# Optimization experiments

Hardware: AMD Instinct MI355X
Metric: run time of the kernel (lower is better)

The kernel has to match this reference:

```python
import jax, jax.numpy as jnp
import numpy as np
from jax import lax

N, D, H, E = 8192, 1024, 4096, 8


def setup_inputs() -> dict:
    key = jax.random.key(0)
    ks = jax.random.split(key, 4)
    return {
        "x": jax.random.normal(ks[0], (N, D), dtype=jnp.float32),
        "wg": jax.random.normal(ks[1], (D, E), dtype=jnp.float32) * 0.001,
        "fc1_w": jax.random.normal(ks[2], (E, D, H), dtype=jnp.float32) * 0.001,
        "fc1_b": jnp.zeros((E, 1, H), dtype=jnp.float32),
        "fc2_w": jax.random.normal(ks[3], (E, H, D), dtype=jnp.float32) * 0.001,
        "fc2_b": jnp.zeros((E, 1, D), dtype=jnp.float32),
        "k": 2,
    }


def reference(x, wg, fc1_w, fc1_b, fc2_w, fc2_b, k):
    n, d = x.shape
    e = wg.shape[1]
    cap = (k * n) // e  # expert capacity (capacity factor 1.0)

    # --- gate ---
    scores = jax.nn.softmax(x @ wg, axis=-1)          # [N,E]
    topv, topi = lax.top_k(scores, k)                 # [N,k]

    # --- top-k routing: position of each (token, slot) within its expert buffer ---
    masks = jax.nn.one_hot(topi, e, dtype=jnp.int32)  # [N,k,E]
    # slot-major priority: all slot-0 assignments before slot-1
    m = jnp.transpose(masks, (1, 0, 2)).reshape(k * n, e)
    pos_flat = jnp.cumsum(m, axis=0) - m              # position before own assignment
    pos = jnp.sum(pos_flat * m, axis=1).reshape(k, n).T   # [N,k]
    valid = pos < cap                                  # capacity overflow -> dropped

    # --- load-balance aux loss (top-1 fraction * mean gate prob) ---
    me = scores.mean(axis=0)                           # [E]
    ce = masks[:, 0, :].astype(scores.dtype).mean(axis=0)
    l_aux = e * jnp.sum(me * ce)

    # --- encode (dispatch): scatter tokens into [E, C, D] buffers ---
    w = valid.astype(x.dtype)                          # [N,k]
    flat_idx = topi * cap + jnp.where(valid, pos, 0)   # [N,k]
    contrib = (x[:, None, :] * w[:, :, None]).reshape(-1, d)
    dispatched = jnp.zeros((e * cap, d), x.dtype).at[flat_idx.reshape(-1)].add(contrib)
    dispatched = dispatched.reshape(e, cap, d)

    # --- batched expert FFN (all-to-all is identity on one device) ---
    h = jax.nn.relu(jnp.einsum('ecd,edh->ech', dispatched, fc1_w) + fc1_b)
    y = jnp.einsum('ech,ehd->ecd', h, fc2_w) + fc2_b   # [E,C,D]

    # --- decode (combine): gather back and weight by gate scores ---
    gathered = y.reshape(e * cap, d)[flat_idx]         # [N,k,D]
    output = jnp.einsum('nk,nkd->nd', topv * w, gathered)
    return output, l_aux
```

## Files before the change

kernel.cpp:

```cpp
#include <hip/hip_runtime.h>
#include <hip/hip_bf16.h>
#include <stdint.h>

#define N_TOK 8192
#define DMODEL 1024
#define HDIM 4096
#define NEXP 8
#define CAP 2048
#define GATE_BLOCKS (N_TOK / 4)

typedef float floatx4 __attribute__((ext_vector_type(4)));
typedef int int32x4_t __attribute__((ext_vector_type(4)));
typedef int int32x8_t __attribute__((ext_vector_type(8)));

static __device__ __forceinline__ void async_copy16(const void* g, void* l) {
  __builtin_amdgcn_global_load_lds(
      (const __attribute__((address_space(1))) void*)g,
      (__attribute__((address_space(3))) void*)l, 16, 0, 0);
}

static __device__ __forceinline__ unsigned int pk4_fp8(float a, float b, float c, float d) {
  int r = __builtin_amdgcn_cvt_pk_fp8_f32(a, b, 0, 0);
  r = __builtin_amdgcn_cvt_pk_fp8_f32(c, d, r, 1);
  return (unsigned int)r;
}

__global__ __launch_bounds__(256) void gate_kernel(
    const float* __restrict__ x, const float* __restrict__ wg,
    float* __restrict__ topv, int* __restrict__ topi,
    float* __restrict__ me_part, int* __restrict__ ce_part) {
  __shared__ float sm_p[4][NEXP];
  __shared__ int sm_i0[4];
  int wave = threadIdx.x >> 6;
  int lane = threadIdx.x & 63;
  int n = blockIdx.x * 4 + wave;
  float acc[NEXP];
#pragma unroll
  for (int e = 0; e < NEXP; e++) acc[e] = 0.f;
  const float* xr = x + (size_t)n * DMODEL;
#pragma unroll 4
  for (int i = 0; i < DMODEL / 64; i++) {
    int idx = lane + 64 * i;
    float xv = xr[idx];
    const float4* wr = (const float4*)(wg + (size_t)idx * NEXP);
    float4 w0 = wr[0], w1 = wr[1];
    acc[0] += xv * w0.x; acc[1] += xv * w0.y;
    acc[2] += xv * w0.z; acc[3] += xv * w0.w;
    acc[4] += xv * w1.x; acc[5] += xv * w1.y;
    acc[6] += xv * w1.z; acc[7] += xv * w1.w;
  }
#pragma unroll
  for (int e = 0; e < NEXP; e++) {
    float v = acc[e];
#pragma unroll
    for (int off = 32; off > 0; off >>= 1) v += __shfl_down(v, off, 64);
    acc[e] = v;
  }
  if (lane == 0) {
    float mx = acc[0];
#pragma unroll
    for (int e = 1; e < NEXP; e++) mx = fmaxf(mx, acc[e]);
    float p[NEXP]; float s = 0.f;
#pragma unroll
    for (int e = 0; e < NEXP; e++) { p[e] = expf(acc[e] - mx); s += p[e]; }
    float inv = 1.f / s;
#pragma unroll
    for (int e = 0; e < NEXP; e++) p[e] *= inv;
    int i0 = 0; float v0 = p[0];
#pragma unroll
    for (int e = 1; e < NEXP; e++) if (p[e] > v0) { v0 = p[e]; i0 = e; }
    int i1 = -1; float v1 = -1.f;
#pragma unroll
    for (int e = 0; e < NEXP; e++) {
      if (e == i0) continue;
      if (p[e] > v1) { v1 = p[e]; i1 = e; }
    }
    topv[n * 2] = v0; topv[n * 2 + 1] = v1;
    topi[n * 2] = i0; topi[n * 2 + 1] = i1;
#pragma unroll
    for (int e = 0; e < NEXP; e++) sm_p[wave][e] = p[e];
    sm_i0[wave] = i0;
  }
  __syncthreads();
  if (threadIdx.x < NEXP) {
    int e = threadIdx.x;
    float pm = 0.f; int cc = 0;
#pragma unroll
    for (int w = 0; w < 4; w++) {
      pm += sm_p[w][e];
      cc += (sm_i0[w] == e) ? 1 : 0;
    }
    me_part[blockIdx.x * NEXP + e] = pm;
    ce_part[blockIdx.x * NEXP + e] = cc;
  }
}

__global__ __launch_bounds__(1024) void scan_kernel(
    const int* __restrict__ topi, const float* __restrict__ topv,
    int* __restrict__ flat_idx, float* __restrict__ cw) {
  __shared__ int hist[16][NEXP];
  __shared__ int base[NEXP];
  int tid = threadIdx.x;
  int w = tid >> 6, lane = tid & 63;
  if (tid < NEXP) base[tid] = 0;
  int vals[16];
#pragma unroll
  for (int c = 0; c < 16; c++) {
    int j = c * 1024 + tid;
    vals[c] = topi[(size_t)(j & 8191) * 2 + (j >> 13)];
  }
  __syncthreads();
  for (int c = 0; c < 16; c++) {
    int j = c * 1024 + tid;
    int slot = j >> 13;
    int n = j & 8191;
    int e = vals[c];
    int rank = 0;
#pragma unroll
    for (int ee = 0; ee < NEXP; ee++) {
      unsigned long long m = __ballot(e == ee);
      if (e == ee) rank = __popcll(m & ((1ull << lane) - 1ull));
      if (lane == ee) hist[w][ee] = __popcll(m);
    }
    __syncthreads();
    if (tid < NEXP) {
      int run = base[tid];
#pragma unroll
      for (int ww = 0; ww < 16; ww++) {
        int t = hist[ww][tid];
        hist[ww][tid] = run;
        run += t;
      }
      base[tid] = run;
    }
    __syncthreads();
    int pos = hist[w][e] + rank;
    bool valid = pos < CAP;
    flat_idx[n * 2 + slot] = e * CAP + (valid ? pos : 0);
    cw[n * 2 + slot] = valid ? topv[n * 2 + slot] : 0.f;
    __syncthreads();
  }
}

__global__ __launch_bounds__(256) void transpose_cvt_fp8(
    const float* __restrict__ in, unsigned char* __restrict__ out,
    int R, int C) {
  __shared__ float tile[32][129];
  const float* inp = in + (size_t)blockIdx.z * R * C;
  unsigned char* outp = out + (size_t)blockIdx.z * R * C;
  int c0 = blockIdx.x * 32, r0 = blockIdx.y * 128;
  int t = threadIdx.x;
#pragma unroll
  for (int p = 0; p < 4; p++) {
    int r = p * 32 + (t >> 3);
    int c4 = (t & 7) * 4;
    float4 v = *(const float4*)(inp + (size_t)(r0 + r) * C + c0 + c4);
    tile[c4 + 0][r] = v.x; tile[c4 + 1][r] = v.y;
    tile[c4 + 2][r] = v.z; tile[c4 + 3][r] = v.w;
  }
  __syncthreads();
  int c = t >> 3, r16 = (t & 7) * 16;
  unsigned int w[4];
#pragma unroll
  for (int j = 0; j < 4; j++) {
    float a = tile[c][r16 + j * 4 + 0] * 512.f;
    float b = tile[c][r16 + j * 4 + 1] * 512.f;
    float cc2 = tile[c][r16 + j * 4 + 2] * 512.f;
    float d = tile[c][r16 + j * 4 + 3] * 512.f;
    w[j] = pk4_fp8(a, b, cc2, d);
  }
  uint4 o; o.x = w[0]; o.y = w[1]; o.z = w[2]; o.w = w[3];
  *(uint4*)(outp + (size_t)(c0 + c) * R + r0 + r16) = o;
}

__global__ __launch_bounds__(64) void dispatch_kernel(
    const float* __restrict__ x, const int* __restrict__ flat_idx,
    const float* __restrict__ cw, unsigned char* __restrict__ disp) {
  int a = blockIdx.x;
  if (cw[a] == 0.f) return;
  int n = a >> 1;
  int f = flat_idx[a];
  int lane = threadIdx.x;
  const float4* xr = (const float4*)(x + (size_t)n * DMODEL);
  unsigned int* dr = (unsigned int*)(disp + (size_t)f * DMODEL);
#pragma unroll
  for (int i = 0; i < 4; i++) {
    float4 v = xr[lane + 64 * i];
    dr[lane + 64 * i] = pk4_fp8(v.x, v.y, v.z, v.w);
  }
}

template <int K_DIM, bool RELU, bool OUT_FP8>
__global__ __launch_bounds__(256) void gemm_fp8_kernel(
    const unsigned char* __restrict__ A, const unsigned char* __restrict__ BT,
    const float* __restrict__ bias, void* __restrict__ Cout, int M, int Ncols,
    float inv_scale, float out_mult) {
  constexpr int BK = 128;
  __shared__ unsigned char As[128 * BK];
  __shared__ unsigned char Bs[128 * BK];
  int e = blockIdx.z;
  int tn = blockIdx.x, tm = blockIdx.y;
  const unsigned char* Ae = A + (size_t)e * M * K_DIM + (size_t)tm * 128 * K_DIM;
  const unsigned char* Be = BT + (size_t)e * Ncols * K_DIM + (size_t)tn * 128 * K_DIM;
  int wv = threadIdx.x >> 6, l = threadIdx.x & 63;
  int wm = wv >> 1, wn = wv & 1;
  int l15 = l & 15, quad = l >> 4;
  int rbase = wv * 8 + (l >> 3);
  int cg = (l & 7) ^ ((l >> 3) & 7);
  floatx4 acc[4][4] = {};
  for (int k0 = 0; k0 < K_DIM; k0 += BK) {
#pragma unroll
    for (int i = 0; i < 4; i++) {
      int r = rbase + i * 32;
      async_copy16(Ae + (size_t)r * K_DIM + k0 + cg * 16, As + i * 4096 + wv * 1024);
      async_copy16(Be + (size_t)r * K_DIM + k0 + cg * 16, Bs + i * 4096 + wv * 1024);
    }
    __syncthreads();
    int32x8_t af[4], bf[4];
#pragma unroll
    for (int mi = 0; mi < 4; mi++) {
      int m = wm * 64 + mi * 16 + l15;
      int x0 = (quad * 2) ^ (m & 7), x1 = (quad * 2 + 1) ^ (m & 7);
      int32x4_t lo = *(const int32x4_t*)(As + m * 128 + x0 * 16);
      int32x4_t hi = *(const int32x4_t*)(As + m * 128 + x1 * 16);
      af[mi] = __builtin_shufflevector(lo, hi, 0, 1, 2, 3, 4, 5, 6, 7);
    }
#pragma unroll
    for (int ni = 0; ni < 4; ni++) {
      int m = wn * 64 + ni * 16 + l15;
      int x0 = (quad * 2) ^ (m & 7), x1 = (quad * 2 + 1) ^ (m & 7);
      int32x4_t lo = *(const int32x4_t*)(Bs + m * 128 + x0 * 16);
      int32x4_t hi = *(const int32x4_t*)(Bs + m * 128 + x1 * 16);
      bf[ni] = __builtin_shufflevector(lo, hi, 0, 1, 2, 3, 4, 5, 6, 7);
    }
#pragma unroll
    for (int mi = 0; mi < 4; mi++)
#pragma unroll
      for (int ni = 0; ni < 4; ni++)
        acc[mi][ni] = __builtin_amdgcn_mfma_scale_f32_16x16x128_f8f6f4(
            af[mi], bf[ni], acc[mi][ni], 0, 0, 0, 0x7F7F7F7F, 0, 0x7F7F7F7F);
    __syncthreads();
  }
  int row_base = tm * 128 + wm * 64;
  int col_base = tn * 128 + wn * 64;
  const float* be = bias + (size_t)e * Ncols;
#pragma unroll
  for (int ni = 0; ni < 4; ni++) {
    int col = col_base + ni * 16 + l15;
    float bv = be[col];
#pragma unroll
    for (int mi = 0; mi < 4; mi++) {
#pragma unroll
      for (int r = 0; r < 4; r++) {
        int row = row_base + mi * 16 + quad * 4 + r;
        float v = acc[mi][ni][r] * inv_scale + bv;
        if (RELU) v = fmaxf(v, 0.f);
        size_t idx = (size_t)e * M * Ncols + (size_t)row * Ncols + col;
        if (OUT_FP8) {
          float s = fminf(fmaxf(v * out_mult, -440.f), 440.f);
          unsigned int b8 = (unsigned int)__builtin_amdgcn_cvt_pk_fp8_f32(s, s, 0, 0) & 0xFF;
          ((unsigned char*)Cout)[idx] = (unsigned char)b8;
        } else {
          ((float*)Cout)[idx] = v;
        }
      }
    }
  }
}

__global__ __launch_bounds__(256) void combine_kernel(
    const float* __restrict__ y, const int* __restrict__ flat_idx,
    const float* __restrict__ cw, float* __restrict__ out) {
  int n = blockIdx.x;
  float w0 = cw[n * 2], w1 = cw[n * 2 + 1];
  int f0 = flat_idx[n * 2], f1 = flat_idx[n * 2 + 1];
  const float4* y0 = (const float4*)(y + (size_t)f0 * DMODEL);
  const float4* y1 = (const float4*)(y + (size_t)f1 * DMODEL);
  float4* o = (float4*)(out + (size_t)n * DMODEL);
  int t = threadIdx.x;
  float4 a = y0[t], b = y1[t];
  float4 r;
  r.x = w0 * a.x + w1 * b.x;
  r.y = w0 * a.y + w1 * b.y;
  r.z = w0 * a.z + w1 * b.z;
  r.w = w0 * a.w + w1 * b.w;
  o[t] = r;
}

__global__ __launch_bounds__(256) void laux_kernel(
    const float* __restrict__ me_part, const int* __restrict__ ce_part,
    float* __restrict__ out_laux) {
  __shared__ float sme[NEXP][33];
  __shared__ float sce[NEXP][33];
  int tid = threadIdx.x;
  int e = tid >> 5;
  int c = tid & 31;
  float pm = 0.f, cc = 0.f;
  for (int b = c; b < GATE_BLOCKS; b += 32) {
    pm += me_part[b * NEXP + e];
    cc += (float)ce_part[b * NEXP + e];
  }
  sme[e][c] = pm;
  sce[e][c] = cc;
  __syncthreads();
  if (tid < NEXP) {
    float tm = 0.f, tc = 0.f;
#pragma unroll
    for (int i = 0; i < 32; i++) { tm += sme[tid][i]; tc += sce[tid][i]; }
    sme[tid][32] = tm;
    sce[tid][32] = tc;
  }
  __syncthreads();
  if (tid == 0) {
    float s = 0.f;
#pragma unroll
    for (int ee = 0; ee < NEXP; ee++)
      s += (sme[ee][32] / (float)N_TOK) * (sce[ee][32] / (float)N_TOK);
    *out_laux = (float)NEXP * s;
  }
}

extern "C" void kernel_launch(void* const* d_in, const int* in_sizes, int n_in,
                              void* d_out, int out_size, void* d_ws,
                              size_t ws_size, hipStream_t stream) {
  (void)in_sizes; (void)n_in; (void)out_size; (void)ws_size;
  const float* x     = (const float*)d_in[0];
  const float* wg    = (const float*)d_in[1];
  const float* fc1_w = (const float*)d_in[2];
  const float* fc1_b = (const float*)d_in[3];
  const float* fc2_w = (const float*)d_in[4];
  const float* fc2_b = (const float*)d_in[5];
  float* out = (float*)d_out;

  char* ws = (char*)d_ws;
  size_t o = 0;
  unsigned char* fc1t = (unsigned char*)(ws + o); o += (size_t)NEXP * DMODEL * HDIM;
  unsigned char* fc2t = (unsigned char*)(ws + o); o += (size_t)NEXP * DMODEL * HDIM;
  unsigned char* disp = (unsigned char*)(ws + o); o += (size_t)NEXP * CAP * DMODEL;
  unsigned char* hbuf = (unsigned char*)(ws + o); o += (size_t)NEXP * CAP * HDIM;
  float* ybuf = (float*)(ws + o); o += (size_t)NEXP * CAP * DMODEL * 4;
  float* topv = (float*)(ws + o); o += (size_t)N_TOK * 2 * 4;
  int* topi   = (int*)(ws + o);   o += (size_t)N_TOK * 2 * 4;
  int* flat   = (int*)(ws + o);   o += (size_t)N_TOK * 2 * 4;
  float* cw   = (float*)(ws + o); o += (size_t)N_TOK * 2 * 4;
  float* mep  = (float*)(ws + o); o += (size_t)GATE_BLOCKS * NEXP * 4;
  int* cep    = (int*)(ws + o);   o += (size_t)GATE_BLOCKS * NEXP * 4;

  hipMemsetAsync(disp, 0, (size_t)NEXP * CAP * DMODEL, stream);

  gate_kernel<<<GATE_BLOCKS, 256, 0, stream>>>(x, wg, topv, topi, mep, cep);
  scan_kernel<<<1, 1024, 0, stream>>>(topi, topv, flat, cw);
  transpose_cvt_fp8<<<dim3(HDIM / 32, DMODEL / 128, NEXP), 256, 0, stream>>>(fc1_w, fc1t, DMODEL, HDIM);
  transpose_cvt_fp8<<<dim3(DMODEL / 32, HDIM / 128, NEXP), 256, 0, stream>>>(fc2_w, fc2t, HDIM, DMODEL);
  dispatch_kernel<<<N_TOK * 2, 64, 0, stream>>>(x, flat, cw, disp);
  gemm_fp8_kernel<DMODEL, true, true>
      <<<dim3(HDIM / 128, CAP / 128, NEXP), 256, 0, stream>>>(
          disp, fc1t, fc1_b, hbuf, CAP, HDIM, 1.f / 512.f, 16.f);
  gemm_fp8_kernel<HDIM, false, false>
      <<<dim3(DMODEL / 128, CAP / 128, NEXP), 256, 0, stream>>>(
          hbuf, fc2t, fc2_b, ybuf, CAP, DMODEL, 1.f / 8192.f, 1.f);
  combine_kernel<<<N_TOK, 256, 0, stream>>>(ybuf, flat, cw, out);
  laux_kernel<<<1, 256, 0, stream>>>(mep, cep, out + (size_t)N_TOK * DMODEL);
}
```

Measured before the change: 627.9 us.

## Load FP8 GEMM fragments straight from global memory with register double-buffering

The expert GEMM no longer stages A and B tiles through LDS with async copies and barriers. Each wave now loads its MFMA fragments straight from global memory into registers, and two register stages are alternated so the next K-slice loads while the current one feeds the MFMAs. This removes the LDS round-trip and the __syncthreads calls, but tiles shared between waves are fetched twice and the kernel relies on L1/L2 for reuse. The zero-fill memset of the dispatch buffer is also removed, so capacity slots that no token fills keep whatever was left in the workspace.

Result: slower. 879.0 us (+40.0%).

```diff
diff --git a/kernel.cpp b/kernel.cpp
--- a/kernel.cpp
+++ b/kernel.cpp
@@ -12,12 +12,6 @@
 typedef float floatx4 __attribute__((ext_vector_type(4)));
 typedef int int32x4_t __attribute__((ext_vector_type(4)));
 typedef int int32x8_t __attribute__((ext_vector_type(8)));
-
-static __device__ __forceinline__ void async_copy16(const void* g, void* l) {
-  __builtin_amdgcn_global_load_lds(
-      (const __attribute__((address_space(1))) void*)g,
-      (__attribute__((address_space(3))) void*)l, 16, 0, 0);
-}
 
 static __device__ __forceinline__ unsigned int pk4_fp8(float a, float b, float c, float d) {
   int r = __builtin_amdgcn_cvt_pk_fp8_f32(a, b, 0, 0);
@@ -195,52 +189,53 @@
     const unsigned char* __restrict__ A, const unsigned char* __restrict__ BT,
     const float* __restrict__ bias, void* __restrict__ Cout, int M, int Ncols,
     float inv_scale, float out_mult) {
-  constexpr int BK = 128;
-  __shared__ unsigned char As[128 * BK];
-  __shared__ unsigned char Bs[128 * BK];
   int e = blockIdx.z;
   int tn = blockIdx.x, tm = blockIdx.y;
-  const unsigned char* Ae = A + (size_t)e * M * K_DIM + (size_t)tm * 128 * K_DIM;
-  const unsigned char* Be = BT + (size_t)e * Ncols * K_DIM + (size_t)tn * 128 * K_DIM;
   int wv = threadIdx.x >> 6, l = threadIdx.x & 63;
   int wm = wv >> 1, wn = wv & 1;
   int l15 = l & 15, quad = l >> 4;
-  int rbase = wv * 8 + (l >> 3);
-  int cg = (l & 7) ^ ((l >> 3) & 7);
+  const unsigned char* Ap =
+      A + ((size_t)e * M + tm * 128 + wm * 64 + l15) * K_DIM + quad * 32;
+  const unsigned char* Bp =
+      BT + ((size_t)e * Ncols + tn * 128 + wn * 64 + l15) * K_DIM + quad * 32;
   floatx4 acc[4][4] = {};
-  for (int k0 = 0; k0 < K_DIM; k0 += BK) {
-#pragma unroll
-    for (int i = 0; i < 4; i++) {
-      int r = rbase + i * 32;
-      async_copy16(Ae + (size_t)r * K_DIM + k0 + cg * 16, As + i * 4096 + wv * 1024);
-      async_copy16(Be + (size_t)r * K_DIM + k0 + cg * 16, Bs + i * 4096 + wv * 1024);
-    }
-    __syncthreads();
-    int32x8_t af[4], bf[4];
-#pragma unroll
-    for (int mi = 0; mi < 4; mi++) {
-      int m = wm * 64 + mi * 16 + l15;
-      int x0 = (quad * 2) ^ (m & 7), x1 = (quad * 2 + 1) ^ (m & 7);
-      int32x4_t lo = *(const int32x4_t*)(As + m * 128 + x0 * 16);
-      int32x4_t hi = *(const int32x4_t*)(As + m * 128 + x1 * 16);
-      af[mi] = __builtin_shufflevector(lo, hi, 0, 1, 2, 3, 4, 5, 6, 7);
-    }
-#pragma unroll
-    for (int ni = 0; ni < 4; ni++) {
-      int m = wn * 64 + ni * 16 + l15;
-      int x0 = (quad * 2) ^ (m & 7), x1 = (quad * 2 + 1) ^ (m & 7);
-      int32x4_t lo = *(const int32x4_t*)(Bs + m * 128 + x0 * 16);
-      int32x4_t hi = *(const int32x4_t*)(Bs + m * 128 + x1 * 16);
-      bf[ni] = __builtin_shufflevector(lo, hi, 0, 1, 2, 3, 4, 5, 6, 7);
-    }
-#pragma unroll
-    for (int mi = 0; mi < 4; mi++)
-#pragma unroll
-      for (int ni = 0; ni < 4; ni++)
-        acc[mi][ni] = __builtin_amdgcn_mfma_scale_f32_16x16x128_f8f6f4(
-            af[mi], bf[ni], acc[mi][ni], 0, 0, 0, 0x7F7F7F7F, 0, 0x7F7F7F7F);
-    __syncthreads();
-  }
+  int32x8_t af[4], bf[4], ag[4], bg[4];
+
+#define LOADF(dst, base, idx, k0)                                              \
+  {                                                                            \
+    const int32x4_t* p =                                                       \
+        (const int32x4_t*)((base) + (size_t)(idx)*16 * K_DIM + (k0));          \
+    int32x4_t lo = p[0];                                                       \
+    int32x4_t hi = p[1];                                                       \
+    dst = __builtin_shufflevector(lo, hi, 0, 1, 2, 3, 4, 5, 6, 7);             \
+  }
+
+#define LOAD_STAGE(a, b, k0)                                                   \
+  {                                                                            \
+    _Pragma("unroll") for (int i = 0; i < 4; i++) LOADF(a[i], Ap, i, k0);      \
+    _Pragma("unroll") for (int i = 0; i < 4; i++) LOADF(b[i], Bp, i, k0);      \
+  }
+
+#define MFMA_STAGE(a, b)                                                       \
+  {                                                                            \
+    _Pragma("unroll") for (int mi = 0; mi < 4; mi++)                           \
+        _Pragma("unroll") for (int ni = 0; ni < 4; ni++) acc[mi][ni] =         \
+        __builtin_amdgcn_mfma_scale_f32_16x16x128_f8f6f4(                      \
+            a[mi], b[ni], acc[mi][ni], 0, 0, 0, 0x7F7F7F7F, 0, 0x7F7F7F7F);    \
+  }
+
+  LOAD_STAGE(af, bf, 0);
+#pragma unroll
+  for (int k0 = 0; k0 < K_DIM; k0 += 256) {
+    LOAD_STAGE(ag, bg, k0 + 128);
+    MFMA_STAGE(af, bf);
+    if (k0 + 256 < K_DIM) LOAD_STAGE(af, bf, k0 + 256);
+    MFMA_STAGE(ag, bg);
+  }
+#undef LOADF
+#undef LOAD_STAGE
+#undef MFMA_STAGE
+
   int row_base = tm * 128 + wm * 64;
   int col_base = tn * 128 + wn * 64;
   const float* be = bias + (size_t)e * Ncols;
@@ -346,7 +341,6 @@
   float* mep  = (float*)(ws + o); o += (size_t)GATE_BLOCKS * NEXP * 4;
   int* cep    = (int*)(ws + o);   o += (size_t)GATE_BLOCKS * NEXP * 4;
 
-  hipMemsetAsync(disp, 0, (size_t)NEXP * CAP * DMODEL, stream);
 
   gate_kernel<<<GATE_BLOCKS, 256, 0, stream>>>(x, wg, topv, topi, mep, cep);
   scan_kernel<<<1, 1024, 0, stream>>>(topi, topv, flat, cw);
```

## Prefetch next GEMM K-stage during MFMA, store FFN output as bf16, drop memset

Applied to the files above, without the earlier changes.

Restructures the fp8 GEMM main loop so each thread loads its A/B fragments from LDS into registers, then issues the async global-to-LDS copies for the next K stage before running the MFMAs. This overlaps global-load latency with compute while keeping a single LDS buffer. The second GEMM now writes its output as bf16 instead of fp32, and the combine kernel reads bf16, which halves the traffic on the intermediate buffer at some precision cost. The memset of the dispatch buffer is removed, because only filled capacity rows are ever gathered.

Measured after the change: 607.7 us. 1.03x faster.

```diff
diff --git a/kernel.cpp b/kernel.cpp
--- a/kernel.cpp
+++ b/kernel.cpp
@@ -23,6 +23,17 @@
   int r = __builtin_amdgcn_cvt_pk_fp8_f32(a, b, 0, 0);
   r = __builtin_amdgcn_cvt_pk_fp8_f32(c, d, r, 1);
   return (unsigned int)r;
+}
+
+static __device__ __forceinline__ unsigned short f2bf(float f) {
+  union { float f; uint32_t u; } v; v.f = f;
+  uint32_t r = (v.u + 0x7FFFu + ((v.u >> 16) & 1u)) >> 16;
+  return (unsigned short)r;
+}
+
+static __device__ __forceinline__ float bf2f(unsigned short u) {
+  union { float f; uint32_t u32; } v; v.u32 = ((uint32_t)u) << 16;
+  return v.f;
 }
 
 __global__ __launch_bounds__(256) void gate_kernel(
@@ -190,12 +201,13 @@
   }
 }
 
-template <int K_DIM, bool RELU, bool OUT_FP8>
+template <int K_DIM, bool RELU, int OUT_MODE>
 __global__ __launch_bounds__(256) void gemm_fp8_kernel(
     const unsigned char* __restrict__ A, const unsigned char* __restrict__ BT,
     const float* __restrict__ bias, void* __restrict__ Cout, int M, int Ncols,
     float inv_scale, float out_mult) {
   constexpr int BK = 128;
+  constexpr int NSTAGE = K_DIM / BK;
   __shared__ unsigned char As[128 * BK];
   __shared__ unsigned char Bs[128 * BK];
   int e = blockIdx.z;
@@ -208,13 +220,21 @@
   int rbase = wv * 8 + (l >> 3);
   int cg = (l & 7) ^ ((l >> 3) & 7);
   floatx4 acc[4][4] = {};
-  for (int k0 = 0; k0 < K_DIM; k0 += BK) {
-#pragma unroll
-    for (int i = 0; i < 4; i++) {
-      int r = rbase + i * 32;
-      async_copy16(Ae + (size_t)r * K_DIM + k0 + cg * 16, As + i * 4096 + wv * 1024);
-      async_copy16(Be + (size_t)r * K_DIM + k0 + cg * 16, Bs + i * 4096 + wv * 1024);
-    }
+
+#define STAGE_LOADS(k0)                                                        \
+  {                                                                            \
+    _Pragma("unroll") for (int i = 0; i < 4; i++) {                            \
+      int r = rbase + i * 32;                                                  \
+      async_copy16(Ae + (size_t)r * K_DIM + (k0) + cg * 16,                    \
+                   As + i * 4096 + wv * 1024);                                 \
+      async_copy16(Be + (size_t)r * K_DIM + (k0) + cg * 16,                    \
+                   Bs + i * 4096 + wv * 1024);                                 \
+    }                                                                          \
+  }
+
+  STAGE_LOADS(0);
+#pragma unroll
+  for (int s = 0; s < NSTAGE; s++) {
     __syncthreads();
     int32x8_t af[4], bf[4];
 #pragma unroll
@@ -233,14 +253,17 @@
       int32x4_t hi = *(const int32x4_t*)(Bs + m * 128 + x1 * 16);
       bf[ni] = __builtin_shufflevector(lo, hi, 0, 1, 2, 3, 4, 5, 6, 7);
     }
+    __syncthreads();
+    if (s + 1 < NSTAGE) STAGE_LOADS((s + 1) * BK);
 #pragma unroll
     for (int mi = 0; mi < 4; mi++)
 #pragma unroll
       for (int ni = 0; ni < 4; ni++)
         acc[mi][ni] = __builtin_amdgcn_mfma_scale_f32_16x16x128_f8f6f4(
             af[mi], bf[ni], acc[mi][ni], 0, 0, 0, 0x7F7F7F7F, 0, 0x7F7F7F7F);
-    __syncthreads();
-  }
+  }
+#undef STAGE_LOADS
+
   int row_base = tm * 128 + wm * 64;
   int col_base = tn * 128 + wn * 64;
   const float* be = bias + (size_t)e * Ncols;
@@ -256,10 +279,12 @@
         float v = acc[mi][ni][r] * inv_scale + bv;
         if (RELU) v = fmaxf(v, 0.f);
         size_t idx = (size_t)e * M * Ncols + (size_t)row * Ncols + col;
-        if (OUT_FP8) {
+        if (OUT_MODE == 1) {
           float s = fminf(fmaxf(v * out_mult, -440.f), 440.f);
           unsigned int b8 = (unsigned int)__builtin_amdgcn_cvt_pk_fp8_f32(s, s, 0, 0) & 0xFF;
           ((unsigned char*)Cout)[idx] = (unsigned char)b8;
+        } else if (OUT_MODE == 2) {
+          ((unsigned short*)Cout)[idx] = f2bf(v);
         } else {
           ((float*)Cout)[idx] = v;
         }
@@ -269,22 +294,24 @@
 }
 
 __global__ __launch_bounds__(256) void combine_kernel(
-    const float* __restrict__ y, const int* __restrict__ flat_idx,
+    const unsigned short* __restrict__ y, const int* __restrict__ flat_idx,
     const float* __restrict__ cw, float* __restrict__ out) {
   int n = blockIdx.x;
   float w0 = cw[n * 2], w1 = cw[n * 2 + 1];
   int f0 = flat_idx[n * 2], f1 = flat_idx[n * 2 + 1];
-  const float4* y0 = (const float4*)(y + (size_t)f0 * DMODEL);
-  const float4* y1 = (const float4*)(y + (size_t)f1 * DMODEL);
-  float4* o = (float4*)(out + (size_t)n * DMODEL);
+  const ushort2* y0 = (const ushort2*)(y + (size_t)f0 * DMODEL);
+  const ushort2* y1 = (const ushort2*)(y + (size_t)f1 * DMODEL);
+  float2* o = (float2*)(out + (size_t)n * DMODEL);
   int t = threadIdx.x;
-  float4 a = y0[t], b = y1[t];
-  float4 r;
-  r.x = w0 * a.x + w1 * b.x;
-  r.y = w0 * a.y + w1 * b.y;
-  r.z = w0 * a.z + w1 * b.z;
-  r.w = w0 * a.w + w1 * b.w;
-  o[t] = r;
+#pragma unroll
+  for (int i = 0; i < 2; i++) {
+    int j = t + i * 256;
+    ushort2 a = y0[j], b = y1[j];
+    float2 r;
+    r.x = w0 * bf2f(a.x) + w1 * bf2f(b.x);
+    r.y = w0 * bf2f(a.y) + w1 * bf2f(b.y);
+    o[j] = r;
+  }
 }
 
 __global__ __launch_bounds__(256) void laux_kernel(
@@ -338,7 +365,7 @@
   unsigned char* fc2t = (unsigned char*)(ws + o); o += (size_t)NEXP * DMODEL * HDIM;
   unsigned char* disp = (unsigned char*)(ws + o); o += (size_t)NEXP * CAP * DMODEL;
   unsigned char* hbuf = (unsigned char*)(ws + o); o += (size_t)NEXP * CAP * HDIM;
-  float* ybuf = (float*)(ws + o); o += (size_t)NEXP * CAP * DMODEL * 4;
+  unsigned short* ybuf = (unsigned short*)(ws + o); o += (size_t)NEXP * CAP * DMODEL * 2;
   float* topv = (float*)(ws + o); o += (size_t)N_TOK * 2 * 4;
   int* topi   = (int*)(ws + o);   o += (size_t)N_TOK * 2 * 4;
   int* flat   = (int*)(ws + o);   o += (size_t)N_TOK * 2 * 4;
@@ -346,17 +373,16 @@
   float* mep  = (float*)(ws + o); o += (size_t)GATE_BLOCKS * NEXP * 4;
   int* cep    = (int*)(ws + o);   o += (size_t)GATE_BLOCKS * NEXP * 4;
 
-  hipMemsetAsync(disp, 0, (size_t)NEXP * CAP * DMODEL, stream);
 
   gate_kernel<<<GATE_BLOCKS, 256, 0, stream>>>(x, wg, topv, topi, mep, cep);
   scan_kernel<<<1, 1024, 0, stream>>>(topi, topv, flat, cw);
   transpose_cvt_fp8<<<dim3(HDIM / 32, DMODEL / 128, NEXP), 256, 0, stream>>>(fc1_w, fc1t, DMODEL, HDIM);
   transpose_cvt_fp8<<<dim3(DMODEL / 32, HDIM / 128, NEXP), 256, 0, stream>>>(fc2_w, fc2t, HDIM, DMODEL);
   dispatch_kernel<<<N_TOK * 2, 64, 0, stream>>>(x, flat, cw, disp);
-  gemm_fp8_kernel<DMODEL, true, true>
+  gemm_fp8_kernel<DMODEL, true, 1>
       <<<dim3(HDIM / 128, CAP / 128, NEXP), 256, 0, stream>>>(
           disp, fc1t, fc1_b, hbuf, CAP, HDIM, 1.f / 512.f, 16.f);
-  gemm_fp8_kernel<HDIM, false, false>
+  gemm_fp8_kernel<HDIM, false, 2>
       <<<dim3(DMODEL / 128, CAP / 128, NEXP), 256, 0, stream>>>(
           hbuf, fc2t, fc2_b, ybuf, CAP, DMODEL, 1.f / 8192.f, 1.f);
   combine_kernel<<<N_TOK, 256, 0, stream>>>(ybuf, flat, cw, out);
```
